# Optimization experiments

Measured on AMD Instinct MI355X. Metric: run time of the kernel, lower is better.

The kernel has to match this reference:

```python
import jax, jax.numpy as jnp
import numpy as np

BS, S, D, H, L, DEG = 16, 512, 256, 4, 6, 16
N = BS * S
E = N * DEG
DH = D // H
LN_EPS = 1e-5


def _ln(x, w, b):
    mu = jnp.mean(x, -1, keepdims=True)
    var = jnp.var(x, -1, keepdims=True)
    return (x - mu) * jax.lax.rsqrt(var + LN_EPS) * w + b


def _gine(x, src, dst, ea, eps, ew, eb, w1, b1, w2, b2):
    # PyG GINEConv: nn((1+eps)*x_i + sum_j relu(x_j + lin(e_ji))), msgs flow src->dst
    msg = jax.nn.relu(x[src] + ea @ ew.T + eb)
    agg = jax.ops.segment_sum(msg, dst, num_segments=x.shape[0])
    z = (1.0 + eps) * x + agg
    return jax.nn.relu(z @ w1.T + b1) @ w2.T + b2


def setup_inputs():
    key = jax.random.key(0)
    ks = iter(jax.random.split(key, 64))
    def rnd(shape, scale=0.05):
        return jax.random.normal(next(ks), shape, jnp.float32) * scale
    rng = np.random.default_rng(0)
    sl = rng.integers(0, S, E)
    dl = rng.integers(0, S, E)
    gid = np.repeat(np.arange(BS), S * DEG)
    edge_index = jnp.asarray(np.stack([sl + gid * S, dl + gid * S]), jnp.int32)
    ptr = jnp.asarray(np.arange(BS + 1) * S, jnp.int32)
    drop_edge_label = jnp.asarray(rng.integers(0, 2, E), jnp.int32)
    return dict(
        x=rnd((N, 2), 1.0),
        edge_attr=jax.random.uniform(next(ks), (E, 1), jnp.float32),
        eps1=jnp.zeros(()), edge_w1=rnd((2, 1)), edge_b1=jnp.zeros((2,)),
        nn1_w1=rnd((64, 2)), nn1_b1=jnp.zeros((64,)),
        nn1_w2=rnd((128, 64)), nn1_b2=jnp.zeros((128,)),
        eps2=jnp.zeros(()), edge_w2=rnd((128, 1)), edge_b2=jnp.zeros((128,)),
        nn2_w1=rnd((D, 128)), nn2_b1=jnp.zeros((D,)),
        nn2_w2=rnd((D, D)), nn2_b2=jnp.zeros((D,)),
        pos_emb=rnd((512, D), 0.02),
        in_proj_w=rnd((L, 3 * D, D)), in_proj_b=jnp.zeros((L, 3 * D)),
        out_proj_w=rnd((L, D, D)), out_proj_b=jnp.zeros((L, D)),
        ln1_w=jnp.ones((L, D)), ln1_b=jnp.zeros((L, D)),
        ln2_w=jnp.ones((L, D)), ln2_b=jnp.zeros((L, D)),
        ff_w1=rnd((L, 2 * D, D)), ff_b1=jnp.zeros((L, 2 * D)),
        ff_w2=rnd((L, D, 2 * D)), ff_b2=jnp.zeros((L, D)),
        fn_w=jnp.ones((D,)), fn_b=jnp.zeros((D,)),
        edge_index=edge_index, ptr=ptr, drop_edge_label=drop_edge_label,
    )


def _forward(x, edge_attr, eps1, edge_w1, edge_b1, nn1_w1, nn1_b1, nn1_w2, nn1_b2,
             eps2, edge_w2, edge_b2, nn2_w1, nn2_b1, nn2_w2, nn2_b2, pos_emb,
             in_proj_w, in_proj_b, out_proj_w, out_proj_b, ln1_w, ln1_b, ln2_w, ln2_b,
             ff_w1, ff_b1, ff_w2, ff_b2, fn_w, fn_b, edge_index, drop_edge_label):
    src, dst = edge_index[0], edge_index[1]
    h = jax.nn.relu(_gine(x, src, dst, edge_attr, eps1, edge_w1, edge_b1,
                          nn1_w1, nn1_b1, nn1_w2, nn1_b2))
    h = _gine(h, src, dst, edge_attr, eps2, edge_w2, edge_b2,
              nn2_w1, nn2_b1, nn2_w2, nn2_b2)
    # equal-size graphs -> batchify is a reshape
    xb = h.reshape(BS, S, D) + pos_emb[:S]
    # graph-derived additive attention mask (src_mask of 1s with 0s at dropped edges,
    # symmetric), plus the float key_padding_mask (all ones here) -- both ADDED to
    # attention logits exactly as torch MultiheadAttention does with float masks.
    g = src // S
    ls = src - g * S
    ld = dst - g * S
    keep = (1 - drop_edge_label).astype(jnp.float32)
    adj = jnp.ones((BS, S, S), jnp.float32)
    adj = adj.at[g, ls, ld].min(keep).at[g, ld, ls].min(keep)
    bias = adj[:, None, :, :] + 1.0  # [BS,1,S,S], broadcast over heads
    scale = 1.0 / jnp.sqrt(jnp.float32(DH))
    for l in range(L):  # norm_first encoder layers, dropout disabled
        hn = _ln(xb, ln1_w[l], ln1_b[l])
        qkv = hn @ in_proj_w[l].T + in_proj_b[l]
        q, k, v = jnp.split(qkv, 3, axis=-1)
        q = q.reshape(BS, S, H, DH).transpose(0, 2, 1, 3)
        k = k.reshape(BS, S, H, DH).transpose(0, 2, 1, 3)
        v = v.reshape(BS, S, H, DH).transpose(0, 2, 1, 3)
        scores = jnp.einsum('bhqd,bhkd->bhqk', q, k) * scale + bias
        attn = jax.nn.softmax(scores, axis=-1)
        o = jnp.einsum('bhqk,bhkd->bhqd', attn, v).transpose(0, 2, 1, 3).reshape(BS, S, D)
        xb = xb + o @ out_proj_w[l].T + out_proj_b[l]
        hn = _ln(xb, ln2_w[l], ln2_b[l])
        xb = xb + jax.nn.silu(hn @ ff_w1[l].T + ff_b1[l]) @ ff_w2[l].T + ff_b2[l]
    return _ln(xb, fn_w, fn_b)


def reference(x, edge_attr, eps1, edge_w1, edge_b1, nn1_w1, nn1_b1, nn1_w2, nn1_b2,
              eps2, edge_w2, edge_b2, nn2_w1, nn2_b1, nn2_w2, nn2_b2, pos_emb,
              in_proj_w, in_proj_b, out_proj_w, out_proj_b, ln1_w, ln1_b, ln2_w, ln2_b,
              ff_w1, ff_b1, ff_w2, ff_b2, fn_w, fn_b, edge_index, ptr, drop_edge_label):
    return _forward(x, edge_attr, eps1, edge_w1, edge_b1, nn1_w1, nn1_b1, nn1_w2, nn1_b2,
                    eps2, edge_w2, edge_b2, nn2_w1, nn2_b1, nn2_w2, nn2_b2, pos_emb,
                    in_proj_w, in_proj_b, out_proj_w, out_proj_b, ln1_w, ln1_b, ln2_w, ln2_b,
                    ff_w1, ff_b1, ff_w2, ff_b2, fn_w, fn_b, edge_index, drop_edge_label)
```

## Files before the change

kernel.cpp:

```cpp
#include <hip/hip_runtime.h>

#define BSZ 16
#define SQ  512
#define DM  256
#define NHD 4
#define NLY 6
#define NND 8192
#define NEG 131072
#define DHD 64

typedef float  f32x4  __attribute__((ext_vector_type(4)));
typedef __bf16 bf16x8 __attribute__((ext_vector_type(8)));

#define N_SRC 31
struct SrcPtrs { const void* p[N_SRC]; };

__device__ __host__ __forceinline__ long asz_at(int i) {
    const int asz[N_SRC] = {16384, 131072, 1, 2, 2, 128, 64, 8192, 128, 1, 128, 128,
                            32768, 256, 65536, 256, 131072, 1179648, 4608, 393216, 1536,
                            1536, 1536, 1536, 1536, 786432, 3072, 786432, 1536, 256, 256};
    return asz[i];
}

__global__ void convert_arena(SrcPtrs sp, __bf16* __restrict__ arena, long total) {
    long gid = (long)blockIdx.x * 256 + threadIdx.x;
    if (gid >= total) return;
    bool isbf = (*(const unsigned int*)sp.p[21]) == 0x3F803F80u;
    long off = 0;
    #pragma unroll
    for (int i = 0; i < N_SRC; i++) {
        long sz = asz_at(i), pad = (sz + 15) & ~15L;
        if (gid >= off && gid < off + sz) {
            long k = gid - off;
            float v = isbf ? (float)((const __bf16*)sp.p[i])[k]
                           : ((const float*)sp.p[i])[k];
            arena[gid] = (__bf16)v;
        }
        off += pad;
    }
}

__global__ void gine1_edge(const __bf16* __restrict__ x, const __bf16* __restrict__ ea,
                           const int* __restrict__ src, const int* __restrict__ dst,
                           const __bf16* __restrict__ ew, const __bf16* __restrict__ eb,
                           float* __restrict__ agg) {
    int e = blockIdx.x * 256 + threadIdx.x;
    if (e >= NEG) return;
    float a = (float)ea[e];
    int s = src[e], d = dst[e];
    float m0 = (float)x[s * 2 + 0] + a * (float)ew[0] + (float)eb[0];
    float m1 = (float)x[s * 2 + 1] + a * (float)ew[1] + (float)eb[1];
    if (m0 > 0.f) atomicAdd(&agg[d * 2 + 0], m0);
    if (m1 > 0.f) atomicAdd(&agg[d * 2 + 1], m1);
}

__global__ void gine1_node(const __bf16* __restrict__ x, const float* __restrict__ agg,
                           const __bf16* __restrict__ eps,
                           const __bf16* __restrict__ w1, const __bf16* __restrict__ b1,
                           const __bf16* __restrict__ w2, const __bf16* __restrict__ b2,
                           float* __restrict__ h1f) {
    __shared__ float hid[2][64];
    int hl = threadIdx.x >> 7, c = threadIdx.x & 127;
    int n = blockIdx.x * 2 + hl;
    float e1 = 1.f + (float)eps[0];
    float z0 = e1 * (float)x[n * 2 + 0] + agg[n * 2 + 0];
    float z1 = e1 * (float)x[n * 2 + 1] + agg[n * 2 + 1];
    if (c < 64) {
        float h = z0 * (float)w1[c * 2 + 0] + z1 * (float)w1[c * 2 + 1] + (float)b1[c];
        hid[hl][c] = h > 0.f ? h : 0.f;
    }
    __syncthreads();
    float s = (float)b2[c];
    #pragma unroll
    for (int h = 0; h < 64; h++) s += hid[hl][h] * (float)w2[c * 64 + h];
    h1f[(long)n * 128 + c] = s > 0.f ? s : 0.f;
}

__global__ void csr_hist(const int* __restrict__ dst, int* __restrict__ deg) {
    int e = blockIdx.x * 256 + threadIdx.x;
    if (e < NEG) atomicAdd(&deg[dst[e]], 1);
}
__global__ void csr_scan(const int* __restrict__ deg, int* __restrict__ ptr) {
    __shared__ int part[256];
    __shared__ int pref[256];
    int t = threadIdx.x, base = t * 32;
    int s = 0;
    for (int i = 0; i < 32; i++) s += deg[base + i];
    part[t] = s;
    __syncthreads();
    if (t == 0) { int run = 0; for (int i = 0; i < 256; i++) { pref[i] = run; run += part[i]; } }
    __syncthreads();
    int run = pref[t];
    for (int i = 0; i < 32; i++) { ptr[base + i] = run; run += deg[base + i]; }
    if (t == 255) ptr[NND] = run;
}
__global__ void csr_copy(const int* __restrict__ ptr, int* __restrict__ pos) {
    int i = blockIdx.x * 256 + threadIdx.x;
    if (i < NND) pos[i] = ptr[i];
}
__global__ void csr_scatter(const int* __restrict__ dst, int* __restrict__ pos,
                            int* __restrict__ elist) {
    int e = blockIdx.x * 256 + threadIdx.x;
    if (e >= NEG) return;
    elist[atomicAdd(&pos[dst[e]], 1)] = e;
}
__global__ __launch_bounds__(128) void gine2_gather(
        const float* __restrict__ h1f, const __bf16* __restrict__ ea,
        const int* __restrict__ src, const int* __restrict__ ptr,
        const int* __restrict__ elist, const __bf16* __restrict__ eps,
        const __bf16* __restrict__ ew, const __bf16* __restrict__ eb,
        __bf16* __restrict__ z2b) {
    int n = blockIdx.x, c = threadIdx.x;
    int beg = ptr[n], end = ptr[n + 1];
    float ewc = (float)ew[c], ebc = (float)eb[c];
    float acc = 0.f;
    for (int j = beg; j < end; j++) {
        int e = elist[j];
        float m = h1f[(long)src[e] * 128 + c] + (float)ea[e] * ewc + ebc;
        acc += m > 0.f ? m : 0.f;
    }
    float e1 = 1.f + (float)eps[0];
    long o = (long)n * 128 + c;
    z2b[o] = (__bf16)(e1 * h1f[o] + acc);
}

__global__ void drop_mask(const int* __restrict__ src, const int* __restrict__ dst,
                          const int* __restrict__ drop, unsigned int* __restrict__ mask) {
    int e = blockIdx.x * 256 + threadIdx.x;
    if (e >= NEG) return;
    if (drop[e]) {
        int s = src[e], d = dst[e];
        int b = s >> 9, ls = s & 511, ld = d & 511;
        atomicOr(&mask[((long)(b * 512 + ls)) * 16 + (ld >> 5)], 1u << (ld & 31));
        atomicOr(&mask[((long)(b * 512 + ld)) * 16 + (ls >> 5)], 1u << (ls & 31));
    }
}

__global__ __launch_bounds__(256) void ln_k(const float* __restrict__ xin,
                                            const __bf16* __restrict__ w,
                                            const __bf16* __restrict__ b,
                                            __bf16* __restrict__ out) {
    int lane = threadIdx.x & 63;
    int row = blockIdx.x * 4 + (threadIdx.x >> 6);
    const float* xr = xin + (long)row * 256;
    f32x4 v = *(const f32x4*)(xr + lane * 4);
    float s  = v[0] + v[1] + v[2] + v[3];
    float s2 = v[0]*v[0] + v[1]*v[1] + v[2]*v[2] + v[3]*v[3];
    #pragma unroll
    for (int o = 32; o > 0; o >>= 1) { s += __shfl_xor(s, o); s2 += __shfl_xor(s2, o); }
    float mean = s * (1.f / 256.f);
    float var  = s2 * (1.f / 256.f) - mean * mean;
    float rstd = rsqrtf(var + 1e-5f);
    __attribute__((aligned(8))) __bf16 o4[4];
    #pragma unroll
    for (int k = 0; k < 4; k++)
        o4[k] = (__bf16)((v[k] - mean) * rstd * (float)w[lane * 4 + k] + (float)b[lane * 4 + k]);
    *(unsigned long long*)(out + (long)row * 256 + lane * 4) = *(const unsigned long long*)o4;
}

__global__ __launch_bounds__(256) void ln_out(const float* __restrict__ xin,
                                              const __bf16* __restrict__ w,
                                              const __bf16* __restrict__ b,
                                              float* __restrict__ out) {
    int lane = threadIdx.x & 63;
    int row = blockIdx.x * 4 + (threadIdx.x >> 6);
    const float* xr = xin + (long)row * 256;
    f32x4 v = *(const f32x4*)(xr + lane * 4);
    float s  = v[0] + v[1] + v[2] + v[3];
    float s2 = v[0]*v[0] + v[1]*v[1] + v[2]*v[2] + v[3]*v[3];
    #pragma unroll
    for (int o = 32; o > 0; o >>= 1) { s += __shfl_xor(s, o); s2 += __shfl_xor(s2, o); }
    float mean = s * (1.f / 256.f);
    float var  = s2 * (1.f / 256.f) - mean * mean;
    float rstd = rsqrtf(var + 1e-5f);
    f32x4 o4;
    #pragma unroll
    for (int k = 0; k < 4; k++)
        o4[k] = (v[k] - mean) * rstd * (float)w[lane * 4 + k] + (float)b[lane * 4 + k];
    *(f32x4*)(out + (long)row * 256 + lane * 4) = o4;
}

__device__ __forceinline__ void gload_lds16(const void* g, void* l) {
    __builtin_amdgcn_global_load_lds(
        (const __attribute__((address_space(1))) void*)g,
        (__attribute__((address_space(3))) void*)l, 16, 0, 0);
}

__device__ __forceinline__ void stage_panel(const __bf16* G, long trow, int K, int k0,
                                            __bf16* panel, int w, int lane) {
    int lin = w * 1024 + lane * 16;
    gload_lds16((const char*)G + ((trow + (lin >> 6)) * K + k0) * 2 + (lin & 63),
                (char*)panel + lin);
}

__global__ __launch_bounds__(256) void gemm_bt(
        const __bf16* __restrict__ A, const __bf16* __restrict__ W,
        const __bf16* __restrict__ bias, __bf16* __restrict__ outb,
        float* __restrict__ outf, const float* __restrict__ resid,
        const __bf16* __restrict__ pos, __bf16* __restrict__ vT,
        int K, int ldout, int act, int qkvmode) {
    __shared__ __attribute__((aligned(16))) __bf16 lA[2][2][64 * 32];
    __shared__ __attribute__((aligned(16))) __bf16 lB[2][2][64 * 32];
    const int tid = threadIdx.x, lane = tid & 63, w = tid >> 6;
    const int wm = w & 1, wn = w >> 1;
    const int quad = lane >> 4, l16 = lane & 15;
    const long tm = (long)blockIdx.x * 64, tn = (long)blockIdx.y * 64;
    f32x4 acc[2][2] = {};
    stage_panel(A, tm, K, 0,  lA[0][0], w, lane);
    stage_panel(A, tm, K, 32, lA[0][1], w, lane);
    stage_panel(W, tn, K, 0,  lB[0][0], w, lane);
    stage_panel(W, tn, K, 32, lB[0][1], w, lane);
    int buf = 0;
    for (int k0 = 0; k0 < K; k0 += 64, buf ^= 1) {
        __syncthreads();
        if (k0 + 64 < K) {
            stage_panel(A, tm, K, k0 + 64, lA[buf ^ 1][0], w, lane);
            stage_panel(A, tm, K, k0 + 96, lA[buf ^ 1][1], w, lane);
            stage_panel(W, tn, K, k0 + 64, lB[buf ^ 1][0], w, lane);
            stage_panel(W, tn, K, k0 + 96, lB[buf ^ 1][1], w, lane);
        }
        const int kg = quad * 8;
        #pragma unroll
        for (int half = 0; half < 2; half++) {
            const __bf16* bA = lA[buf][half];
            const __bf16* bB = lB[buf][half];
            bf16x8 af[2], bfv[2];
            #pragma unroll
            for (int i = 0; i < 2; i++) af[i]  = *(const bf16x8*)&bA[(wm * 32 + i * 16 + l16) * 32 + kg];
            #pragma unroll
            for (int j = 0; j < 2; j++) bfv[j] = *(const bf16x8*)&bB[(wn * 32 + j * 16 + l16) * 32 + kg];
            #pragma unroll
            for (int i = 0; i < 2; i++)
                #pragma unroll
                for (int j = 0; j < 2; j++)
                    acc[i][j] = __builtin_amdgcn_mfma_f32_16x16x32_bf16(af[i], bfv[j], acc[i][j], 0, 0, 0);
        }
    }
    #pragma unroll
    for (int i = 0; i < 2; i++) {
        #pragma unroll
        for (int j = 0; j < 2; j++) {
            #pragma unroll
            for (int r = 0; r < 4; r++) {
                int m = (int)tm + wm * 32 + i * 16 + quad * 4 + r;
                int n = (int)tn + wn * 32 + j * 16 + l16;
                float v = acc[i][j][r];
                if (bias) v += (float)bias[n];
                if (act == 1) v = v > 0.f ? v : 0.f;
                else if (act == 2) v = v / (1.f + __expf(-v));
                if (qkvmode) {
                    if (n < 512) {
                        if (n < 256) v *= 0.125f;
                        outb[(long)m * ldout + n] = (__bf16)v;
                    } else {
                        int vc = n - 512, hh = vc >> 6, d = vc & 63;
                        int b = m >> 9, sdx = m & 511;
                        vT[(((long)(b * NHD + hh) * DHD + d) << 9) + sdx] = (__bf16)v;
                    }
                } else if (outf) {
                    if (resid) v += resid[(long)m * ldout + n];
                    if (pos)   v += (float)pos[(long)(m & 511) * ldout + n];
                    outf[(long)m * ldout + n] = v;
                } else {
                    outb[(long)m * ldout + n] = (__bf16)v;
                }
            }
        }
    }
}

#define PSTR 40
__global__ __launch_bounds__(64) void attn_fused(const __bf16* __restrict__ qk,
                                                 const __bf16* __restrict__ vT,
                                                 const unsigned int* __restrict__ mask,
                                                 __bf16* __restrict__ attno) {
    __shared__ __bf16 pt[16 * PSTR];
    const int lane = threadIdx.x;
    const int qb = blockIdx.x, h = blockIdx.y, b = blockIdx.z;
    const int qr0 = qb * 16;
    const int quad = lane >> 4, l16 = lane & 15;
    const int bh = b * NHD + h;
    const __bf16* qbase = qk + ((long)(b * 512 + qr0 + l16)) * 512 + h * 64 + quad * 8;
    bf16x8 qf0 = *(const bf16x8*)(qbase);
    bf16x8 qf1 = *(const bf16x8*)(qbase + 32);
    const unsigned int* mrow = mask + ((long)(b * 512 + qr0 + quad * 4)) * 16;
    f32x4 O[4] = {};
    float lsum[4] = {0.f, 0.f, 0.f, 0.f};
    #pragma unroll 4
    for (int c = 0; c < 512; c += 32) {
        f32x4 s[2];
        #pragma unroll
        for (int tt = 0; tt < 2; tt++) {
            const __bf16* kbase = qk + ((long)(b * 512 + c + tt * 16 + l16)) * 512 + 256 + h * 64 + quad * 8;
            bf16x8 kf0 = *(const bf16x8*)(kbase);
            bf16x8 kf1 = *(const bf16x8*)(kbase + 32);
            f32x4 z = {0.f, 0.f, 0.f, 0.f};
            z = __builtin_amdgcn_mfma_f32_16x16x32_bf16(qf0, kf0, z, 0, 0, 0);
            s[tt] = __builtin_amdgcn_mfma_f32_16x16x32_bf16(qf1, kf1, z, 0, 0, 0);
        }
        #pragma unroll
        for (int tt = 0; tt < 2; tt++)
            #pragma unroll
            for (int r = 0; r < 4; r++) {
                unsigned int wd = mrow[r * 16 + (c >> 5)];
                float bias = 2.f - (float)((wd >> (tt * 16 + l16)) & 1u);
                float e = __expf(s[tt][r] + bias);
                lsum[r] += e;
                pt[(quad * 4 + r) * PSTR + tt * 16 + l16] = (__bf16)e;
            }
        bf16x8 pf = *(const bf16x8*)&pt[l16 * PSTR + quad * 8];
        #pragma unroll
        for (int j = 0; j < 4; j++) {
            const __bf16* vrow = vT + ((long)bh * 64 + j * 16 + l16) * 512 + c + quad * 8;
            bf16x8 vf = *(const bf16x8*)(vrow);
            O[j] = __builtin_amdgcn_mfma_f32_16x16x32_bf16(pf, vf, O[j], 0, 0, 0);
        }
    }
    #pragma unroll
    for (int r = 0; r < 4; r++)
        #pragma unroll
        for (int o = 1; o < 16; o <<= 1) lsum[r] += __shfl_xor(lsum[r], o);
    float inv[4];
    #pragma unroll
    for (int r = 0; r < 4; r++) inv[r] = 1.f / lsum[r];
    #pragma unroll
    for (int j = 0; j < 4; j++)
        #pragma unroll
        for (int r = 0; r < 4; r++) {
            int m = qr0 + quad * 4 + r, d = j * 16 + l16;
            attno[((long)(b * 512 + m)) * 256 + h * 64 + d] = (__bf16)(O[j][r] * inv[r]);
        }
}

extern "C" void kernel_launch(void* const* d_in, const int* in_sizes, int n_in,
                              void* d_out, int out_size, void* d_ws, size_t ws_size,
                              hipStream_t stream) {
    const long MB = 1024 * 1024;

    const int* ei   = (const int*)d_in[31];
    const int* drop = (const int*)d_in[33];
    const int* esrc = ei;
    const int* edst = ei + NEG;

    char* ws = (char*)d_ws;
    float*  xb    = (float*)(ws + 0);
    __bf16* arena = (__bf16*)(ws + 8 * MB);
    unsigned int* maskw = (unsigned int*)(ws + 15 * MB + 512 * 1024);
    float*  agg1  = (float*)(ws + 16 * MB);
    int*    deg   = (int*)(ws + 17 * MB);
    int*    ptrc  = (int*)(ws + 17 * MB + 64 * 1024);
    int*    posc  = (int*)(ws + 17 * MB + 128 * 1024);
    int*    elist = (int*)(ws + 17 * MB + 192 * 1024);
    float*  h1f   = (float*)(ws + 21 * MB);
    __bf16* z2b   = (__bf16*)(ws + 25 * MB);
    __bf16* t1b   = (__bf16*)(ws + 27 * MB);
    __bf16* hnb   = (__bf16*)(ws + 31 * MB);
    __bf16* qkb   = (__bf16*)(ws + 35 * MB);
    __bf16* vT    = (__bf16*)(ws + 43 * MB);
    __bf16* attno = (__bf16*)(ws + 47 * MB);
    __bf16* ff1b  = (__bf16*)(ws + 51 * MB);

    SrcPtrs sp;
    __bf16* ap[N_SRC];
    long off = 0;
    for (int i = 0; i < N_SRC; i++) {
        sp.p[i] = d_in[i];
        ap[i] = arena + off;
        off += (asz_at(i) + 15) & ~15L;
    }
    convert_arena<<<(int)((off + 255) / 256), 256, 0, stream>>>(sp, arena, off);

    const __bf16 *xA = ap[0], *eaA = ap[1], *eps1A = ap[2], *ew1A = ap[3], *eb1A = ap[4],
                 *n1w1A = ap[5], *n1b1A = ap[6], *n1w2A = ap[7], *n1b2A = ap[8],
                 *eps2A = ap[9], *ew2A = ap[10], *eb2A = ap[11],
                 *n2w1A = ap[12], *n2b1A = ap[13], *n2w2A = ap[14], *n2b2A = ap[15],
                 *posA = ap[16], *ipwA = ap[17], *ipbA = ap[18], *opwA = ap[19], *opbA = ap[20],
                 *ln1wA = ap[21], *ln1bA = ap[22], *ln2wA = ap[23], *ln2bA = ap[24],
                 *f1wA = ap[25], *f1bA = ap[26], *f2wA = ap[27], *f2bA = ap[28],
                 *fnwA = ap[29], *fnbA = ap[30];

    hipMemsetAsync(agg1, 0, (size_t)NND * 2 * 4, stream);
    hipMemsetAsync(deg, 0, (size_t)NND * 4, stream);
    hipMemsetAsync(maskw, 0, (size_t)512 * 1024, stream);

    csr_hist<<<NEG / 256, 256, 0, stream>>>(edst, deg);
    csr_scan<<<1, 256, 0, stream>>>(deg, ptrc);
    csr_copy<<<NND / 256, 256, 0, stream>>>(ptrc, posc);
    csr_scatter<<<NEG / 256, 256, 0, stream>>>(edst, posc, elist);

    gine1_edge<<<NEG / 256, 256, 0, stream>>>(xA, eaA, esrc, edst, ew1A, eb1A, agg1);
    gine1_node<<<NND / 2, 256, 0, stream>>>(xA, agg1, eps1A, n1w1A, n1b1A, n1w2A, n1b2A, h1f);
    gine2_gather<<<NND, 128, 0, stream>>>(h1f, eaA, esrc, ptrc, elist, eps2A, ew2A, eb2A, z2b);

    gemm_bt<<<dim3(NND / 64, 4), 256, 0, stream>>>(z2b, n2w1A, n2b1A, t1b, nullptr, nullptr, nullptr, nullptr,
                                                   128, 256, 1, 0);
    gemm_bt<<<dim3(NND / 64, 4), 256, 0, stream>>>(t1b, n2w2A, n2b2A, nullptr, xb, nullptr, posA, nullptr,
                                                   256, 256, 0, 0);

    drop_mask<<<NEG / 256, 256, 0, stream>>>(esrc, edst, drop, maskw);

    for (int l = 0; l < NLY; l++) {
        ln_k<<<NND / 4, 256, 0, stream>>>(xb, ln1wA + l * 256, ln1bA + l * 256, hnb);
        gemm_bt<<<dim3(NND / 64, 12), 256, 0, stream>>>(hnb, ipwA + (long)l * 768 * 256, ipbA + l * 768,
                                                        qkb, nullptr, nullptr, nullptr, vT,
                                                        256, 512, 0, 1);
        attn_fused<<<dim3(32, NHD, BSZ), 64, 0, stream>>>(qkb, vT, maskw, attno);
        gemm_bt<<<dim3(NND / 64, 4), 256, 0, stream>>>(attno, opwA + (long)l * 256 * 256, opbA + l * 256,
                                                       nullptr, xb, xb, nullptr, nullptr,
                                                       256, 256, 0, 0);
        ln_k<<<NND / 4, 256, 0, stream>>>(xb, ln2wA + l * 256, ln2bA + l * 256, hnb);
        gemm_bt<<<dim3(NND / 64, 8), 256, 0, stream>>>(hnb, f1wA + (long)l * 512 * 256, f1bA + l * 512,
                                                       ff1b, nullptr, nullptr, nullptr, nullptr,
                                                       256, 512, 2, 0);
        gemm_bt<<<dim3(NND / 64, 4), 256, 0, stream>>>(ff1b, f2wA + (long)l * 256 * 512, f2bA + l * 256,
                                                       nullptr, xb, xb, nullptr, nullptr,
                                                       512, 256, 0, 0);
    }
    ln_out<<<NND / 4, 256, 0, stream>>>(xb, fnwA, fnbA, (float*)d_out);
}
```

Before: 832.3 us.

## Template GEMM on K, shrink K-step to 32, fold CSR copy into scan

```diff
diff --git a/kernel.cpp b/kernel.cpp
--- a/kernel.cpp
+++ b/kernel.cpp
@@ -80,7 +80,8 @@
     int e = blockIdx.x * 256 + threadIdx.x;
     if (e < NEG) atomicAdd(&deg[dst[e]], 1);
 }
-__global__ void csr_scan(const int* __restrict__ deg, int* __restrict__ ptr) {
+__global__ void csr_scan(const int* __restrict__ deg, int* __restrict__ ptr,
+                         int* __restrict__ pos) {
     __shared__ int part[256];
     __shared__ int pref[256];
     int t = threadIdx.x, base = t * 32;
@@ -91,12 +92,8 @@
     if (t == 0) { int run = 0; for (int i = 0; i < 256; i++) { pref[i] = run; run += part[i]; } }
     __syncthreads();
     int run = pref[t];
-    for (int i = 0; i < 32; i++) { ptr[base + i] = run; run += deg[base + i]; }
+    for (int i = 0; i < 32; i++) { ptr[base + i] = run; pos[base + i] = run; run += deg[base + i]; }
     if (t == 255) ptr[NND] = run;
-}
-__global__ void csr_copy(const int* __restrict__ ptr, int* __restrict__ pos) {
-    int i = blockIdx.x * 256 + threadIdx.x;
-    if (i < NND) pos[i] = ptr[i];
 }
 __global__ void csr_scatter(const int* __restrict__ dst, int* __restrict__ pos,
                             int* __restrict__ elist) {
@@ -186,55 +183,50 @@
         (__attribute__((address_space(3))) void*)l, 16, 0, 0);
 }
 
-__device__ __forceinline__ void stage_panel(const __bf16* G, long trow, int K, int k0,
-                                            __bf16* panel, int w, int lane) {
+__device__ __forceinline__ void stage_tile64(const __bf16* A, const __bf16* W,
+                                             long tm, long tn, int K, int k0,
+                                             __bf16* bA, __bf16* bB, int w, int lane) {
     int lin = w * 1024 + lane * 16;
-    gload_lds16((const char*)G + ((trow + (lin >> 6)) * K + k0) * 2 + (lin & 63),
-                (char*)panel + lin);
-}
-
+    gload_lds16((const char*)A + ((tm + (lin >> 6)) * K + k0) * 2 + (lin & 63),
+                (char*)bA + lin);
+    gload_lds16((const char*)W + ((tn + (lin >> 6)) * K + k0) * 2 + (lin & 63),
+                (char*)bB + lin);
+}
+
+template <int K>
 __global__ __launch_bounds__(256) void gemm_bt(
         const __bf16* __restrict__ A, const __bf16* __restrict__ W,
         const __bf16* __restrict__ bias, __bf16* __restrict__ outb,
         float* __restrict__ outf, const float* __restrict__ resid,
         const __bf16* __restrict__ pos, __bf16* __restrict__ vT,
-        int K, int ldout, int act, int qkvmode) {
-    __shared__ __attribute__((aligned(16))) __bf16 lA[2][2][64 * 32];
-    __shared__ __attribute__((aligned(16))) __bf16 lB[2][2][64 * 32];
+        int ldout, int act, int qkvmode) {
+    __shared__ __attribute__((aligned(16))) __bf16 lA[2][64 * 32];
+    __shared__ __attribute__((aligned(16))) __bf16 lB[2][64 * 32];
     const int tid = threadIdx.x, lane = tid & 63, w = tid >> 6;
     const int wm = w & 1, wn = w >> 1;
     const int quad = lane >> 4, l16 = lane & 15;
     const long tm = (long)blockIdx.x * 64, tn = (long)blockIdx.y * 64;
     f32x4 acc[2][2] = {};
-    stage_panel(A, tm, K, 0,  lA[0][0], w, lane);
-    stage_panel(A, tm, K, 32, lA[0][1], w, lane);
-    stage_panel(W, tn, K, 0,  lB[0][0], w, lane);
-    stage_panel(W, tn, K, 32, lB[0][1], w, lane);
-    int buf = 0;
-    for (int k0 = 0; k0 < K; k0 += 64, buf ^= 1) {
+    stage_tile64(A, W, tm, tn, K, 0, lA[0], lB[0], w, lane);
+    #pragma unroll
+    for (int k0 = 0; k0 < K; k0 += 32) {
+        const int buf = (k0 >> 5) & 1;
         __syncthreads();
-        if (k0 + 64 < K) {
-            stage_panel(A, tm, K, k0 + 64, lA[buf ^ 1][0], w, lane);
-            stage_panel(A, tm, K, k0 + 96, lA[buf ^ 1][1], w, lane);
-            stage_panel(W, tn, K, k0 + 64, lB[buf ^ 1][0], w, lane);
-            stage_panel(W, tn, K, k0 + 96, lB[buf ^ 1][1], w, lane);
-        }
+        if (k0 + 32 < K)
+            stage_tile64(A, W, tm, tn, K, k0 + 32, lA[buf ^ 1], lB[buf ^ 1], w, lane);
+        const __bf16* bA = lA[buf];
+        const __bf16* bB = lB[buf];
         const int kg = quad * 8;
-        #pragma unroll
-        for (int half = 0; half < 2; half++) {
-            const __bf16* bA = lA[buf][half];
-            const __bf16* bB = lB[buf][half];
-            bf16x8 af[2], bfv[2];
+        bf16x8 af[2], bfv[2];
+        #pragma unroll
+        for (int i = 0; i < 2; i++) af[i]  = *(const bf16x8*)&bA[(wm * 32 + i * 16 + l16) * 32 + kg];
+        #pragma unroll
+        for (int j = 0; j < 2; j++) bfv[j] = *(const bf16x8*)&bB[(wn * 32 + j * 16 + l16) * 32 + kg];
+        #pragma unroll
+        for (int i = 0; i < 2; i++)
             #pragma unroll
-            for (int i = 0; i < 2; i++) af[i]  = *(const bf16x8*)&bA[(wm * 32 + i * 16 + l16) * 32 + kg];
-            #pragma unroll
-            for (int j = 0; j < 2; j++) bfv[j] = *(const bf16x8*)&bB[(wn * 32 + j * 16 + l16) * 32 + kg];
-            #pragma unroll
-            for (int i = 0; i < 2; i++)
-                #pragma unroll
-                for (int j = 0; j < 2; j++)
-                    acc[i][j] = __builtin_amdgcn_mfma_f32_16x16x32_bf16(af[i], bfv[j], acc[i][j], 0, 0, 0);
-        }
+            for (int j = 0; j < 2; j++)
+                acc[i][j] = __builtin_amdgcn_mfma_f32_16x16x32_bf16(af[i], bfv[j], acc[i][j], 0, 0, 0);
     }
     #pragma unroll
     for (int i = 0; i < 2; i++) {
@@ -345,20 +337,20 @@
     char* ws = (char*)d_ws;
     float*  xb    = (float*)(ws + 0);
     __bf16* arena = (__bf16*)(ws + 8 * MB);
-    unsigned int* maskw = (unsigned int*)(ws + 15 * MB + 512 * 1024);
-    float*  agg1  = (float*)(ws + 16 * MB);
-    int*    deg   = (int*)(ws + 17 * MB);
-    int*    ptrc  = (int*)(ws + 17 * MB + 64 * 1024);
-    int*    posc  = (int*)(ws + 17 * MB + 128 * 1024);
-    int*    elist = (int*)(ws + 17 * MB + 192 * 1024);
-    float*  h1f   = (float*)(ws + 21 * MB);
-    __bf16* z2b   = (__bf16*)(ws + 25 * MB);
-    __bf16* t1b   = (__bf16*)(ws + 27 * MB);
-    __bf16* hnb   = (__bf16*)(ws + 31 * MB);
-    __bf16* qkb   = (__bf16*)(ws + 35 * MB);
-    __bf16* vT    = (__bf16*)(ws + 43 * MB);
-    __bf16* attno = (__bf16*)(ws + 47 * MB);
-    __bf16* ff1b  = (__bf16*)(ws + 51 * MB);
+    unsigned int* maskw = (unsigned int*)(ws + 16 * MB);
+    float*  agg1  = (float*)(ws + 17 * MB);
+    int*    deg   = (int*)(ws + 18 * MB);
+    int*    ptrc  = (int*)(ws + 18 * MB + 64 * 1024);
+    int*    posc  = (int*)(ws + 18 * MB + 128 * 1024);
+    int*    elist = (int*)(ws + 18 * MB + 192 * 1024);
+    float*  h1f   = (float*)(ws + 19 * MB);
+    __bf16* z2b   = (__bf16*)(ws + 23 * MB);
+    __bf16* t1b   = (__bf16*)(ws + 25 * MB);
+    __bf16* hnb   = (__bf16*)(ws + 29 * MB);
+    __bf16* qkb   = (__bf16*)(ws + 33 * MB);
+    __bf16* vT    = (__bf16*)(ws + 41 * MB);
+    __bf16* attno = (__bf16*)(ws + 45 * MB);
+    __bf16* ff1b  = (__bf16*)(ws + 49 * MB);
 
     SrcPtrs sp;
     __bf16* ap[N_SRC];
@@ -384,37 +376,36 @@
     hipMemsetAsync(maskw, 0, (size_t)512 * 1024, stream);
 
     csr_hist<<<NEG / 256, 256, 0, stream>>>(edst, deg);
-    csr_scan<<<1, 256, 0, stream>>>(deg, ptrc);
-    csr_copy<<<NND / 256, 256, 0, stream>>>(ptrc, posc);
+    csr_scan<<<1, 256, 0, stream>>>(deg, ptrc, posc);
     csr_scatter<<<NEG / 256, 256, 0, stream>>>(edst, posc, elist);
 
     gine1_edge<<<NEG / 256, 256, 0, stream>>>(xA, eaA, esrc, edst, ew1A, eb1A, agg1);
     gine1_node<<<NND / 2, 256, 0, stream>>>(xA, agg1, eps1A, n1w1A, n1b1A, n1w2A, n1b2A, h1f);
     gine2_gather<<<NND, 128, 0, stream>>>(h1f, eaA, esrc, ptrc, elist, eps2A, ew2A, eb2A, z2b);
 
-    gemm_bt<<<dim3(NND / 64, 4), 256, 0, stream>>>(z2b, n2w1A, n2b1A, t1b, nullptr, nullptr, nullptr, nullptr,
-                                                   128, 256, 1, 0);
-    gemm_bt<<<dim3(NND / 64, 4), 256, 0, stream>>>(t1b, n2w2A, n2b2A, nullptr, xb, nullptr, posA, nullptr,
-                                                   256, 256, 0, 0);
+    gemm_bt<128><<<dim3(NND / 64, 4), 256, 0, stream>>>(z2b, n2w1A, n2b1A, t1b, nullptr, nullptr, nullptr, nullptr,
+                                                        256, 1, 0);
+    gemm_bt<256><<<dim3(NND / 64, 4), 256, 0, stream>>>(t1b, n2w2A, n2b2A, nullptr, xb, nullptr, posA, nullptr,
+                                                        256, 0, 0);
 
     drop_mask<<<NEG / 256, 256, 0, stream>>>(esrc, edst, drop, maskw);
 
     for (int l = 0; l < NLY; l++) {
         ln_k<<<NND / 4, 256, 0, stream>>>(xb, ln1wA + l * 256, ln1bA + l * 256, hnb);
-        gemm_bt<<<dim3(NND / 64, 12), 256, 0, stream>>>(hnb, ipwA + (long)l * 768 * 256, ipbA + l * 768,
-                                                        qkb, nullptr, nullptr, nullptr, vT,
-                                                        256, 512, 0, 1);
+        gemm_bt<256><<<dim3(NND / 64, 12), 256, 0, stream>>>(hnb, ipwA + (long)l * 768 * 256, ipbA + l * 768,
+                                                             qkb, nullptr, nullptr, nullptr, vT,
+                                                             512, 0, 1);
         attn_fused<<<dim3(32, NHD, BSZ), 64, 0, stream>>>(qkb, vT, maskw, attno);
-        gemm_bt<<<dim3(NND / 64, 4), 256, 0, stream>>>(attno, opwA + (long)l * 256 * 256, opbA + l * 256,
-                                                       nullptr, xb, xb, nullptr, nullptr,
-                                                       256, 256, 0, 0);
+        gemm_bt<256><<<dim3(NND / 64, 4), 256, 0, stream>>>(attno, opwA + (long)l * 256 * 256, opbA + l * 256,
+                                                            nullptr, xb, xb, nullptr, nullptr,
+                                                            256, 0, 0);
         ln_k<<<NND / 4, 256, 0, stream>>>(xb, ln2wA + l * 256, ln2bA + l * 256, hnb);
-        gemm_bt<<<dim3(NND / 64, 8), 256, 0, stream>>>(hnb, f1wA + (long)l * 512 * 256, f1bA + l * 512,
-                                                       ff1b, nullptr, nullptr, nullptr, nullptr,
-                                                       256, 512, 2, 0);
-        gemm_bt<<<dim3(NND / 64, 4), 256, 0, stream>>>(ff1b, f2wA + (long)l * 256 * 512, f2bA + l * 256,
-                                                       nullptr, xb, xb, nullptr, nullptr,
-                                                       512, 256, 0, 0);
+        gemm_bt<256><<<dim3(NND / 64, 8), 256, 0, stream>>>(hnb, f1wA + (long)l * 512 * 256, f1bA + l * 512,
+                                                            ff1b, nullptr, nullptr, nullptr, nullptr,
+                                                            512, 2, 0);
+        gemm_bt<512><<<dim3(NND / 64, 4), 256, 0, stream>>>(ff1b, f2wA + (long)l * 256 * 512, f2bA + l * 256,
+                                                            nullptr, xb, xb, nullptr, nullptr,
+                                                            256, 0, 0);
     }
     ln_out<<<NND / 4, 256, 0, stream>>>(xb, fnwA, fnbA, (float*)d_out);
 }
```

After: 818.9 us. No clear change (-1.6%).
